# Kernel optimization log

Measured on AMD Instinct MI355X. Metric: run time of the kernel, lower is better.

## Reference

```python
import jax, jax.numpy as jnp
import numpy as np
from jax import lax

IN_CH = 512
OUT_CH = 512
KERNEL = 3
STYLE_DIM = 512
BATCH = 8
HW = 64
EPS = 1e-08
LR_MUL = 1.0


def setup_inputs() -> dict:
    key = jax.random.key(0)
    k1, k2, k3, k4 = jax.random.split(key, 4)
    x = jax.random.normal(k1, (BATCH, IN_CH, HW, HW), dtype=jnp.float32)
    style = jax.random.normal(k2, (BATCH, STYLE_DIM), dtype=jnp.float32)
    weight = jax.random.normal(k3, (1, OUT_CH, IN_CH, KERNEL, KERNEL), dtype=jnp.float32)
    mod_weight = jax.random.normal(k4, (IN_CH, STYLE_DIM), dtype=jnp.float32)
    mod_bias = jnp.ones((IN_CH,), dtype=jnp.float32)  # bias_init=1
    return {"x": x, "style": style, "weight": weight,
            "mod_weight": mod_weight, "mod_bias": mod_bias}


def reference(x, style, weight, mod_weight, mod_bias):
    batch, in_ch, h, w_dim = x.shape
    conv_scale = 1.0 / np.sqrt(in_ch * KERNEL * KERNEL)
    lin_scale = 1.0 / np.sqrt(STYLE_DIM) * LR_MUL

    # EqualizedLinear modulation: style -> per-channel scale, shape (B, in_ch)
    s = style @ (mod_weight * lin_scale).T + mod_bias * LR_MUL

    # Modulate: (B, out, in, k, k)
    w = conv_scale * weight * s[:, None, :, None, None]
    # Demodulate
    demod = lax.rsqrt(jnp.sum(w * w, axis=(2, 3, 4)) + EPS)  # (B, out)
    w = w * demod[:, :, None, None, None]

    pad = KERNEL // 2

    def conv_one(xi, wi):
        # xi: (in, H, W), wi: (out, in, k, k)
        return lax.conv_general_dilated(
            xi[None], wi, window_strides=(1, 1),
            padding=[(pad, pad), (pad, pad)],
            dimension_numbers=("NCHW", "OIHW", "NCHW"))[0]

    out = jax.vmap(conv_one)(x, w)  # (B, out, H, W)
    return out
```

## Files before the change

kernel.cpp:

```cpp
#include <hip/hip_runtime.h>
#include <hip/hip_bf16.h>
#include <cstdint>

#define IN_CH 512
#define OUT_CH 512
#define STYLE_DIM 512
#define BATCH 8
#define HW 64

typedef __bf16 bf16x8 __attribute__((ext_vector_type(8)));
typedef float f32x16 __attribute__((ext_vector_type(16)));

__device__ __forceinline__ void gload_lds16(const void* g, void* l) {
  __builtin_amdgcn_global_load_lds(
      (const __attribute__((address_space(1))) unsigned int*)g,
      (__attribute__((address_space(3))) unsigned int*)l,
      16, 0, 0);
}

#define WAITV(N) asm volatile("s_waitcnt vmcnt(" #N ")" ::: "memory")
#define BARRIER() do { asm volatile("" ::: "memory"); __builtin_amdgcn_s_barrier(); \
                       asm volatile("" ::: "memory"); } while (0)

__global__ void k_style(const float* __restrict__ style, const float* __restrict__ modw,
                        const float* __restrict__ modb, float* __restrict__ s_out,
                        float* __restrict__ zpg) {
  const int tid = threadIdx.x;
  if (blockIdx.x == 128) {
    float4 z = {0.f, 0.f, 0.f, 0.f};
    #pragma unroll
    for (int k = 0; k < 4; ++k) ((float4*)zpg)[tid * 4 + k] = z;
    return;
  }
  __shared__ float st[BATCH * STYLE_DIM];
  for (int i = tid; i < BATCH * STYLE_DIM; i += 256) st[i] = style[i];
  __syncthreads();
  const int ic = blockIdx.x * 4 + (tid >> 6);
  const int l = tid & 63;
  const float* mr = modw + (size_t)ic * STYLE_DIM + l * 8;
  float m[8];
  #pragma unroll
  for (int j = 0; j < 8; ++j) m[j] = mr[j];
  float accs[8];
  #pragma unroll
  for (int b = 0; b < 8; ++b) {
    const float* sb = st + b * STYLE_DIM + l * 8;
    float a = 0.f;
    #pragma unroll
    for (int j = 0; j < 8; ++j) a += m[j] * sb[j];
    accs[b] = a;
  }
  #pragma unroll
  for (int off = 32; off; off >>= 1) {
    #pragma unroll
    for (int b = 0; b < 8; ++b) accs[b] += __shfl_down(accs[b], off, 64);
  }
  if (l == 0) {
    #pragma unroll
    for (int b = 0; b < 8; ++b)
      s_out[b * IN_CH + ic] = accs[b] * 0.04419417382415922f + modb[ic];
  }
}

__global__ void k_prep(const float* __restrict__ x, const float* __restrict__ s,
                       const float* __restrict__ w,
                       __bf16* __restrict__ xgp, __bf16* __restrict__ wgp,
                       float* __restrict__ scale) {
  const int t = threadIdx.x;
  const int bid = blockIdx.x;
  if (bid < 512) {
    const int b = bid >> 6, y = bid & 63;
    const int xcol = t & 63;
    const int g0 = t >> 6;
    const float* sr = s + b * IN_CH;
    const size_t rowbase = ((size_t)(b * 64 + y)) * 8 * 528;
    #pragma unroll
    for (int i = 0; i < 8; ++i) {
      const int g = i * 8 + g0;
      bf16x8 pk;
      #pragma unroll
      for (int e = 0; e < 8; ++e) {
        const int ic = g * 8 + e;
        pk[e] = (__bf16)(x[(((size_t)(b * IN_CH) + ic) * HW + y) * HW + xcol] * sr[ic]);
      }
      const int col = xcol + 1, c = col >> 1;
      const int p = 2 * (((g & 7) + c) & 7) + (col & 1);
      *(bf16x8*)(xgp + (rowbase + (size_t)(g >> 3) * 528 + c * 16 + p) * 8) = pk;
    }
    if (t < 128) {
      const int col = (t & 1) * 65, g = t >> 1;
      const int c = col >> 1;
      const int p = 2 * (((g & 7) + c) & 7) + (col & 1);
      bf16x8 z = {};
      *(bf16x8*)(xgp + (rowbase + (size_t)(g >> 3) * 528 + c * 16 + p) * 8) = z;
    }
  } else if (bid < 1024) {
    const int idx = (bid - 512) * 512 + t;
    const int oc = idx >> 9, ic = idx & 511;
    const int octile = oc >> 8, R = oc & 255, j = R >> 1;
    const int chunk = ic >> 6, sslot = (ic >> 3) & 7, e = ic & 7;
    const int p = 2 * ((sslot + j) & 7) + (R & 1);
    const int u = j * 16 + p;
    const float* pw = w + ((size_t)oc * IN_CH + ic) * 9;
    #pragma unroll
    for (int tp = 0; tp < 9; ++tp)
      wgp[((size_t)((tp * 8 + chunk) * 2 + octile) * 2048 + u) * 8 + e] = (__bf16)pw[tp];
  } else {
    const int oc = (bid - 1024) * 8 + (t >> 6);
    const int l = t & 63;
    float w8[8];
    #pragma unroll
    for (int j = 0; j < 8; ++j) {
      const float* pw = w + ((size_t)oc * IN_CH + l * 8 + j) * 9;
      float sum = 0.f;
      #pragma unroll
      for (int tp = 0; tp < 9; ++tp) { float v = pw[tp]; sum += v * v; }
      w8[j] = sum;
    }
    #pragma unroll
    for (int b = 0; b < 8; ++b) {
      const float* sb = s + b * IN_CH + l * 8;
      float acc = 0.f;
      #pragma unroll
      for (int j = 0; j < 8; ++j) { float sv = sb[j]; acc += sv * sv * w8[j]; }
      #pragma unroll
      for (int off = 32; off; off >>= 1) acc += __shfl_down(acc, off, 64);
      if (l == 0)
        scale[b * OUT_CH + oc] =
            rsqrtf(acc * (1.0f / 4608.0f) + 1e-8f) * 0.014731391274719732f;
    }
  }
}

__global__ __launch_bounds__(512, 2) void k_conv(
    const __bf16* __restrict__ Wgp,
    const __bf16* __restrict__ Xgp,
    const float* __restrict__ scale,
    const __bf16* __restrict__ zpg,
    float* __restrict__ out)
{
  __shared__ __attribute__((aligned(16))) __bf16 Xs[3584 * 8];
  __shared__ __attribute__((aligned(16))) __bf16 Wl[3][2048 * 8];

  const int tid = threadIdx.x;
  const int lane = tid & 63;
  const int wid = tid >> 6;
  const int wm = wid >> 2;
  const int wn = wid & 3;
  const int ln31 = lane & 31;
  const int laneK = lane >> 5;
  const int kord = wid & 3;

  const int bid0 = blockIdx.x;
  const int bid = (bid0 & 7) * 32 + (bid0 >> 3);
  const int octile = bid & 1;
  const int ptile = (bid >> 1) & 15;
  const int b = bid >> 5;
  const int r0 = ptile * 4;
  const int oc0 = octile * 256;

  auto stage_w = [&](int chunkv, int tapv, int bsel) {
    const __bf16* base = Wgp + (size_t)((tapv * 8 + chunkv) * 2 + octile) * (2048 * 8);
    #pragma unroll
    for (int i = 0; i < 4; ++i) {
      const int u = i * 512 + tid;
      gload_lds16(base + (size_t)u * 8, (void*)((char*)Wl[bsel] + u * 16));
    }
  };
  auto stage_x = [&](int chunkv) {
    #pragma unroll
    for (int i = 0; i < 7; ++i) {
      const unsigned u = i * 512 + tid;
      const unsigned row = u / 528u;
      const unsigned rr = u - row * 528u;
      const int y = r0 - 1 + (int)row;
      const bool ok = (u < 3168u) & (y >= 0) & (y < HW);
      const __bf16* src = ok
          ? Xgp + (((size_t)(b * 64 + y) * 8 + chunkv) * 528 + rr) * 8
          : zpg;
      gload_lds16(src, (void*)((char*)Xs + u * 16));
    }
  };

  stage_x(0);
  stage_w(0, 0, 0);
  stage_w(0, 1, 1);

  int aoffR[4];
  #pragma unroll
  for (int i = 0; i < 4; ++i)
    aoffR[i] = ((ln31 + 4 * (kord + i) + 2 * laneK) & 15) * 8;
  int beleR[3][4];
  #pragma unroll
  for (int dxi = 0; dxi < 3; ++dxi) {
    const int col = ln31 + dxi, c = col >> 1;
    #pragma unroll
    for (int i = 0; i < 4; ++i) {
      const int pos = (col & 1) + 2 * ((2 * (kord + i) + laneK + c) & 7);
      beleR[dxi][i] = c * 128 + pos * 8;
    }
  }
  const __bf16* __restrict__ ab0 = Wl[0] + (64 * wm + (ln31 >> 1)) * 128;
  const __bf16* __restrict__ ab1 = Wl[1] + (64 * wm + (ln31 >> 1)) * 128;
  const __bf16* __restrict__ ab2 = Wl[2] + (64 * wm + (ln31 >> 1)) * 128;

  f32x16 acc[4][2] = {};
  bf16x8 bvp0, bvp1;

#define TAPBODY(T) { \
    if ((T) == 8 && c == 7) { WAITV(0); } else { WAITV(4); } \
    BARRIER(); \
    const __bf16* __restrict__ abase = ((T) % 3 == 0) ? ab0 : ((T) % 3 == 1) ? ab1 : ab2; \
    const __bf16* __restrict__ xbase = Xs + (wn + (T) / 3) * (33 * 128); \
    _Pragma("unroll") \
    for (int i = 0; i < 4; ++i) { \
      const int ael = aoffR[i]; \
      const int bel = beleR[(T) % 3][i]; \
      bf16x8 av[4], bv[2]; \
      _Pragma("unroll") \
      for (int mf = 0; mf < 4; ++mf) av[mf] = *(const bf16x8*)(abase + mf * 2048 + ael); \
      if ((T) > 0 && i == 0) { bv[0] = bvp0; bv[1] = bvp1; } \
      else { bv[0] = *(const bf16x8*)(xbase + bel); \
             bv[1] = *(const bf16x8*)(xbase + 2048 + bel); } \
      _Pragma("unroll") \
      for (int mf = 0; mf < 4; ++mf) { \
        acc[mf][0] = __builtin_amdgcn_mfma_f32_32x32x16_bf16(av[mf], bv[0], acc[mf][0], 0, 0, 0); \
        acc[mf][1] = __builtin_amdgcn_mfma_f32_32x32x16_bf16(av[mf], bv[1], acc[mf][1], 0, 0, 0); \
      } \
    } \
    if ((T) < 8) {    \
      const __bf16* __restrict__ xn = Xs + (wn + ((T) + 1) / 3) * (33 * 128); \
      const int beln = beleR[((T) + 1) % 3][0]; \
      bvp0 = *(const bf16x8*)(xn + beln); \
      bvp1 = *(const bf16x8*)(xn + 2048 + beln); \
    } \
    if ((T) == 8) { \
      if (c < 7) { BARRIER(); stage_x(c + 1); stage_w(c + 1, 1, 1); } \
    } else if ((T) <= 6) { \
      stage_w(c, (T) + 2, ((T) + 2) % 3); \
    } else {  \
      if (c < 7) stage_w(c + 1, 0, 0); \
    } \
  }

  #pragma unroll 1
  for (int c = 0; c < 8; ++c) {
    TAPBODY(0) TAPBODY(1) TAPBODY(2)
    TAPBODY(3) TAPBODY(4) TAPBODY(5)
    TAPBODY(6) TAPBODY(7) TAPBODY(8)
  }

  const int y = r0 + wn;
  #pragma unroll
  for (int mf = 0; mf < 4; ++mf) {
    #pragma unroll
    for (int reg = 0; reg < 16; ++reg) {
      const int rowid = (reg & 3) + 8 * (reg >> 2) + 4 * laneK;
      const int oc = oc0 + 128 * wm + 32 * mf + rowid;
      const float sc = scale[b * OUT_CH + oc];
      float* op = out + (((size_t)(b * OUT_CH + oc) * HW + y) * HW) + ln31;
      op[0] = acc[mf][0][reg] * sc;
      op[32] = acc[mf][1][reg] * sc;
    }
  }
}

extern "C" void kernel_launch(void* const* d_in, const int* in_sizes, int n_in,
                              void* d_out, int out_size, void* d_ws, size_t ws_size,
                              hipStream_t stream) {
  const float* x      = (const float*)d_in[0];
  const float* style  = (const float*)d_in[1];
  const float* weight = (const float*)d_in[2];
  const float* modw   = (const float*)d_in[3];
  const float* modb   = (const float*)d_in[4];
  float* out = (float*)d_out;

  char* ws = (char*)d_ws;
  float*  s_buf = (float*)(ws + 0);
  float*  scale = (float*)(ws + 16384);
  __bf16* zpg   = (__bf16*)(ws + 32768);
  __bf16* wgp   = (__bf16*)(ws + 49152);
  __bf16* xgp   = (__bf16*)(ws + 49152 + 9 * 8 * 2 * 2048 * 8 * 2);

  k_style<<<129, 256, 0, stream>>>(style, modw, modb, s_buf, (float*)zpg);
  k_prep<<<1088, 512, 0, stream>>>(x, s_buf, weight, xgp, wgp, scale);
  k_conv<<<256, 512, 0, stream>>>(wgp, xgp, scale, zpg, out);
}
```

Measured before the change: 160.5 us.

## Shrink conv tile to 128 OC with 32-channel K chunks and 4-wave blocks

Reorganizes the implicit-GEMM conv so each block covers 128 output channels with 4 waves (instead of 256 OC with 8 waves), using 32-input-channel chunks instead of 64. The grid doubles to 512 blocks, and the packed X and W layouts in the prep kernel get matching new swizzles. The goal is better occupancy and load balance across the CUs by using smaller LDS tiles. The cost is twice as many barrier-separated K steps, more re-reads of X per output channel, and removal of the B-fragment prefetch across taps.

```diff
diff --git a/kernel.cpp b/kernel.cpp
--- a/kernel.cpp
+++ b/kernel.cpp
@@ -73,7 +73,7 @@
     const int xcol = t & 63;
     const int g0 = t >> 6;
     const float* sr = s + b * IN_CH;
-    const size_t rowbase = ((size_t)(b * 64 + y)) * 8 * 528;
+    const size_t rowbase = ((size_t)(b * 64 + y)) * 16 * 272;
     #pragma unroll
     for (int i = 0; i < 8; ++i) {
       const int g = i * 8 + g0;
@@ -83,28 +83,32 @@
         const int ic = g * 8 + e;
         pk[e] = (__bf16)(x[(((size_t)(b * IN_CH) + ic) * HW + y) * HW + xcol] * sr[ic]);
       }
-      const int col = xcol + 1, c = col >> 1;
-      const int p = 2 * (((g & 7) + c) & 7) + (col & 1);
-      *(bf16x8*)(xgp + (rowbase + (size_t)(g >> 3) * 528 + c * 16 + p) * 8) = pk;
-    }
-    if (t < 128) {
-      const int col = (t & 1) * 65, g = t >> 1;
-      const int c = col >> 1;
-      const int p = 2 * (((g & 7) + c) & 7) + (col & 1);
+      const int col = xcol + 1, c4 = col >> 2;
+      const int p = (col & 3) + 4 * (((g & 3) + c4) & 3);
+      *(bf16x8*)(xgp + (rowbase + (size_t)(g >> 2) * 272 + c4 * 16 + p) * 8) = pk;
+    }
+    if (t < 256) {
+      const int hc = t & 3;
+      const int col = hc ? 64 + hc : 0;
+      const int g = t >> 2;
+      const int c4 = col >> 2;
+      const int p = (col & 3) + 4 * (((g & 3) + c4) & 3);
       bf16x8 z = {};
-      *(bf16x8*)(xgp + (rowbase + (size_t)(g >> 3) * 528 + c * 16 + p) * 8) = z;
+      *(bf16x8*)(xgp + (rowbase + (size_t)(g >> 2) * 272 + c4 * 16 + p) * 8) = z;
     }
   } else if (bid < 1024) {
     const int idx = (bid - 512) * 512 + t;
     const int oc = idx >> 9, ic = idx & 511;
-    const int octile = oc >> 8, R = oc & 255, j = R >> 1;
-    const int chunk = ic >> 6, sslot = (ic >> 3) & 7, e = ic & 7;
-    const int p = 2 * ((sslot + j) & 7) + (R & 1);
+    const int octile = oc >> 7;
+    const int R = oc & 127, j = R >> 2, r = R & 3;
+    const int chunk = ic >> 5;
+    const int sl = (ic >> 3) & 3, e = ic & 7;
+    const int p = r + 4 * ((sl + j) & 3);
     const int u = j * 16 + p;
     const float* pw = w + ((size_t)oc * IN_CH + ic) * 9;
     #pragma unroll
     for (int tp = 0; tp < 9; ++tp)
-      wgp[((size_t)((tp * 8 + chunk) * 2 + octile) * 2048 + u) * 8 + e] = (__bf16)pw[tp];
+      wgp[((size_t)((tp * 16 + chunk) * 4 + octile) * 512 + u) * 8 + e] = (__bf16)pw[tp];
   } else {
     const int oc = (bid - 1024) * 8 + (t >> 6);
     const int l = t & 63;
@@ -132,51 +136,49 @@
   }
 }
 
-__global__ __launch_bounds__(512, 2) void k_conv(
+__global__ __launch_bounds__(256, 2) void k_conv(
     const __bf16* __restrict__ Wgp,
     const __bf16* __restrict__ Xgp,
     const float* __restrict__ scale,
     const __bf16* __restrict__ zpg,
     float* __restrict__ out)
 {
-  __shared__ __attribute__((aligned(16))) __bf16 Xs[3584 * 8];
-  __shared__ __attribute__((aligned(16))) __bf16 Wl[3][2048 * 8];
+  __shared__ __attribute__((aligned(16))) __bf16 Xs[1792 * 8];
+  __shared__ __attribute__((aligned(16))) __bf16 Wl[3][512 * 8];
 
   const int tid = threadIdx.x;
   const int lane = tid & 63;
-  const int wid = tid >> 6;
-  const int wm = wid >> 2;
-  const int wn = wid & 3;
+  const int wn = tid >> 6;
   const int ln31 = lane & 31;
   const int laneK = lane >> 5;
-  const int kord = wid & 3;
 
   const int bid0 = blockIdx.x;
-  const int bid = (bid0 & 7) * 32 + (bid0 >> 3);
-  const int octile = bid & 1;
-  const int ptile = (bid >> 1) & 15;
-  const int b = bid >> 5;
+  const int bid = (bid0 & 7) * 64 + (bid0 >> 3);
+  const int b = bid >> 6;
+  const int rem = bid & 63;
+  const int ptile = rem >> 2;
+  const int octile = rem & 3;
   const int r0 = ptile * 4;
-  const int oc0 = octile * 256;
+  const int oc0 = octile * 128;
 
   auto stage_w = [&](int chunkv, int tapv, int bsel) {
-    const __bf16* base = Wgp + (size_t)((tapv * 8 + chunkv) * 2 + octile) * (2048 * 8);
-    #pragma unroll
-    for (int i = 0; i < 4; ++i) {
-      const int u = i * 512 + tid;
+    const __bf16* base = Wgp + (size_t)((tapv * 16 + chunkv) * 4 + octile) * (512 * 8);
+    #pragma unroll
+    for (int i = 0; i < 2; ++i) {
+      const int u = i * 256 + tid;
       gload_lds16(base + (size_t)u * 8, (void*)((char*)Wl[bsel] + u * 16));
     }
   };
   auto stage_x = [&](int chunkv) {
     #pragma unroll
     for (int i = 0; i < 7; ++i) {
-      const unsigned u = i * 512 + tid;
-      const unsigned row = u / 528u;
-      const unsigned rr = u - row * 528u;
+      const unsigned u = i * 256 + tid;
+      const unsigned row = u / 272u;
+      const unsigned rr = u - row * 272u;
       const int y = r0 - 1 + (int)row;
-      const bool ok = (u < 3168u) & (y >= 0) & (y < HW);
+      const bool ok = (u < 1632u) & (y >= 0) & (y < HW);
       const __bf16* src = ok
-          ? Xgp + (((size_t)(b * 64 + y) * 8 + chunkv) * 528 + rr) * 8
+          ? Xgp + (((size_t)(b * 64 + y) * 16 + chunkv) * 272 + rr) * 8
           : zpg;
       gload_lds16(src, (void*)((char*)Xs + u * 16));
     }
@@ -186,65 +188,58 @@
   stage_w(0, 0, 0);
   stage_w(0, 1, 1);
 
-  int aoffR[4];
-  #pragma unroll
-  for (int i = 0; i < 4; ++i)
-    aoffR[i] = ((ln31 + 4 * (kord + i) + 2 * laneK) & 15) * 8;
-  int beleR[3][4];
+  int aoffR[2];
+  #pragma unroll
+  for (int ksl = 0; ksl < 2; ++ksl)
+    aoffR[ksl] = ((ln31 + 8 * ksl + 4 * laneK) & 15) * 8;
+  int beleR[3][2];
   #pragma unroll
   for (int dxi = 0; dxi < 3; ++dxi) {
-    const int col = ln31 + dxi, c = col >> 1;
-    #pragma unroll
-    for (int i = 0; i < 4; ++i) {
-      const int pos = (col & 1) + 2 * ((2 * (kord + i) + laneK + c) & 7);
-      beleR[dxi][i] = c * 128 + pos * 8;
-    }
-  }
-  const __bf16* __restrict__ ab0 = Wl[0] + (64 * wm + (ln31 >> 1)) * 128;
-  const __bf16* __restrict__ ab1 = Wl[1] + (64 * wm + (ln31 >> 1)) * 128;
-  const __bf16* __restrict__ ab2 = Wl[2] + (64 * wm + (ln31 >> 1)) * 128;
+    const int col = ln31 + dxi;
+    const int c4 = col >> 2;
+    #pragma unroll
+    for (int ksl = 0; ksl < 2; ++ksl) {
+      const int pos = (col + 8 * ksl + 4 * laneK) & 15;
+      beleR[dxi][ksl] = c4 * 128 + pos * 8;
+    }
+  }
+  const __bf16* __restrict__ ab0 = Wl[0] + (ln31 >> 2) * 128;
+  const __bf16* __restrict__ ab1 = Wl[1] + (ln31 >> 2) * 128;
+  const __bf16* __restrict__ ab2 = Wl[2] + (ln31 >> 2) * 128;
 
   f32x16 acc[4][2] = {};
-  bf16x8 bvp0, bvp1;
 
 #define TAPBODY(T) { \
-    if ((T) == 8 && c == 7) { WAITV(0); } else { WAITV(4); } \
+    if ((T) == 8 && c == 15) { WAITV(0); } else { WAITV(2); } \
     BARRIER(); \
     const __bf16* __restrict__ abase = ((T) % 3 == 0) ? ab0 : ((T) % 3 == 1) ? ab1 : ab2; \
-    const __bf16* __restrict__ xbase = Xs + (wn + (T) / 3) * (33 * 128); \
+    const __bf16* __restrict__ xbase = Xs + (wn + (T) / 3) * 2176; \
     _Pragma("unroll") \
-    for (int i = 0; i < 4; ++i) { \
-      const int ael = aoffR[i]; \
-      const int bel = beleR[(T) % 3][i]; \
+    for (int ksl = 0; ksl < 2; ++ksl) { \
+      const int ael = aoffR[ksl]; \
+      const int bel = beleR[(T) % 3][ksl]; \
       bf16x8 av[4], bv[2]; \
       _Pragma("unroll") \
-      for (int mf = 0; mf < 4; ++mf) av[mf] = *(const bf16x8*)(abase + mf * 2048 + ael); \
-      if ((T) > 0 && i == 0) { bv[0] = bvp0; bv[1] = bvp1; } \
-      else { bv[0] = *(const bf16x8*)(xbase + bel); \
-             bv[1] = *(const bf16x8*)(xbase + 2048 + bel); } \
+      for (int mf = 0; mf < 4; ++mf) av[mf] = *(const bf16x8*)(abase + mf * 1024 + ael); \
+      bv[0] = *(const bf16x8*)(xbase + bel); \
+      bv[1] = *(const bf16x8*)(xbase + 1024 + bel); \
       _Pragma("unroll") \
       for (int mf = 0; mf < 4; ++mf) { \
         acc[mf][0] = __builtin_amdgcn_mfma_f32_32x32x16_bf16(av[mf], bv[0], acc[mf][0], 0, 0, 0); \
         acc[mf][1] = __builtin_amdgcn_mfma_f32_32x32x16_bf16(av[mf], bv[1], acc[mf][1], 0, 0, 0); \
       } \
     } \
-    if ((T) < 8) {    \
-      const __bf16* __restrict__ xn = Xs + (wn + ((T) + 1) / 3) * (33 * 128); \
-      const int beln = beleR[((T) + 1) % 3][0]; \
-      bvp0 = *(const bf16x8*)(xn + beln); \
-      bvp1 = *(const bf16x8*)(xn + 2048 + beln); \
-    } \
     if ((T) == 8) { \
-      if (c < 7) { BARRIER(); stage_x(c + 1); stage_w(c + 1, 1, 1); } \
+      if (c < 15) { BARRIER(); stage_x(c + 1); stage_w(c + 1, 1, 1); } \
     } else if ((T) <= 6) { \
       stage_w(c, (T) + 2, ((T) + 2) % 3); \
     } else {  \
-      if (c < 7) stage_w(c + 1, 0, 0); \
+      if (c < 15) stage_w(c + 1, 0, 0); \
     } \
   }
 
   #pragma unroll 1
-  for (int c = 0; c < 8; ++c) {
+  for (int c = 0; c < 16; ++c) {
     TAPBODY(0) TAPBODY(1) TAPBODY(2)
     TAPBODY(3) TAPBODY(4) TAPBODY(5)
     TAPBODY(6) TAPBODY(7) TAPBODY(8)
@@ -256,7 +251,7 @@
     #pragma unroll
     for (int reg = 0; reg < 16; ++reg) {
       const int rowid = (reg & 3) + 8 * (reg >> 2) + 4 * laneK;
-      const int oc = oc0 + 128 * wm + 32 * mf + rowid;
+      const int oc = oc0 + 32 * mf + rowid;
       const float sc = scale[b * OUT_CH + oc];
       float* op = out + (((size_t)(b * OUT_CH + oc) * HW + y) * HW) + ln31;
       op[0] = acc[mf][0][reg] * sc;
@@ -280,9 +275,9 @@
   float*  scale = (float*)(ws + 16384);
   __bf16* zpg   = (__bf16*)(ws + 32768);
   __bf16* wgp   = (__bf16*)(ws + 49152);
-  __bf16* xgp   = (__bf16*)(ws + 49152 + 9 * 8 * 2 * 2048 * 8 * 2);
+  __bf16* xgp   = (__bf16*)(ws + 49152 + 9 * 16 * 4 * 512 * 16);
 
   k_style<<<129, 256, 0, stream>>>(style, modw, modb, s_buf, (float*)zpg);
   k_prep<<<1088, 512, 0, stream>>>(x, s_buf, weight, xgp, wgp, scale);
-  k_conv<<<256, 512, 0, stream>>>(wgp, xgp, scale, zpg, out);
-}
+  k_conv<<<512, 256, 0, stream>>>(wgp, xgp, scale, zpg, out);
+}
```

After: 160.9 us. Within noise of the previous version (+0.2%).

## Load conv input operands straight from global memory instead of staging in LDS

Applied to the files above, without the earlier changes.

The conv kernel stops staging the input tile in shared memory and has each wave read its B-operand fragments directly from a new padded global layout, with the top and bottom halo rows pre-zeroed by extra blocks in the style kernel. Weight staging becomes a uniform rolling schedule across chunks, which removes the extra per-chunk barrier and the input restaging step. This frees LDS and cuts barrier stalls, but in exchange each wave issues more global or L2 loads and has no explicit software prefetch for X, so latency has to be hidden by the wait placement and by occupancy.

```diff
diff --git a/kernel.cpp b/kernel.cpp
--- a/kernel.cpp
+++ b/kernel.cpp
@@ -22,14 +22,28 @@
 #define BARRIER() do { asm volatile("" ::: "memory"); __builtin_amdgcn_s_barrier(); \
                        asm volatile("" ::: "memory"); } while (0)
 
+#define XSLOT 528
+#define XROW  4224
+#define XCHUNK (66 * 4224)
+
 __global__ void k_style(const float* __restrict__ style, const float* __restrict__ modw,
                         const float* __restrict__ modb, float* __restrict__ s_out,
-                        float* __restrict__ zpg) {
+                        __bf16* __restrict__ xgp) {
   const int tid = threadIdx.x;
-  if (blockIdx.x == 128) {
-    float4 z = {0.f, 0.f, 0.f, 0.f};
-    #pragma unroll
-    for (int k = 0; k < 4; ++k) ((float4*)zpg)[tid * 4 + k] = z;
+  if (blockIdx.x >= 128) {
+    const int b = blockIdx.x - 128;
+    bf16x8 z = {};
+    #pragma unroll
+    for (int it = 0; it < 33; ++it) {
+      const int u = it * 256 + tid;
+      const int chunk = u / 1056;
+      const int rem = u - chunk * 1056;
+      const int yidx = (rem / 528) * 65;
+      const int rem2 = rem % 528;
+      const int slot = rem2 / 66, col = rem2 % 66;
+      *(bf16x8*)(xgp + ((size_t)(b * 8 + chunk) * XCHUNK + (size_t)yidx * XROW
+                        + slot * XSLOT + col * 8)) = z;
+    }
     return;
   }
   __shared__ float st[BATCH * STYLE_DIM];
@@ -73,7 +87,6 @@
     const int xcol = t & 63;
     const int g0 = t >> 6;
     const float* sr = s + b * IN_CH;
-    const size_t rowbase = ((size_t)(b * 64 + y)) * 8 * 528;
     #pragma unroll
     for (int i = 0; i < 8; ++i) {
       const int g = i * 8 + g0;
@@ -83,16 +96,14 @@
         const int ic = g * 8 + e;
         pk[e] = (__bf16)(x[(((size_t)(b * IN_CH) + ic) * HW + y) * HW + xcol] * sr[ic]);
       }
-      const int col = xcol + 1, c = col >> 1;
-      const int p = 2 * (((g & 7) + c) & 7) + (col & 1);
-      *(bf16x8*)(xgp + (rowbase + (size_t)(g >> 3) * 528 + c * 16 + p) * 8) = pk;
+      *(bf16x8*)(xgp + ((size_t)(b * 8 + (g >> 3)) * XCHUNK + (size_t)(y + 1) * XROW
+                        + (g & 7) * XSLOT + (xcol + 1) * 8)) = pk;
     }
     if (t < 128) {
       const int col = (t & 1) * 65, g = t >> 1;
-      const int c = col >> 1;
-      const int p = 2 * (((g & 7) + c) & 7) + (col & 1);
       bf16x8 z = {};
-      *(bf16x8*)(xgp + (rowbase + (size_t)(g >> 3) * 528 + c * 16 + p) * 8) = z;
+      *(bf16x8*)(xgp + ((size_t)(b * 8 + (g >> 3)) * XCHUNK + (size_t)(y + 1) * XROW
+                        + (g & 7) * XSLOT + col * 8)) = z;
     }
   } else if (bid < 1024) {
     const int idx = (bid - 512) * 512 + t;
@@ -136,10 +147,8 @@
     const __bf16* __restrict__ Wgp,
     const __bf16* __restrict__ Xgp,
     const float* __restrict__ scale,
-    const __bf16* __restrict__ zpg,
     float* __restrict__ out)
 {
-  __shared__ __attribute__((aligned(16))) __bf16 Xs[3584 * 8];
   __shared__ __attribute__((aligned(16))) __bf16 Wl[3][2048 * 8];
 
   const int tid = threadIdx.x;
@@ -149,7 +158,6 @@
   const int wn = wid & 3;
   const int ln31 = lane & 31;
   const int laneK = lane >> 5;
-  const int kord = wid & 3;
 
   const int bid0 = blockIdx.x;
   const int bid = (bid0 & 7) * 32 + (bid0 >> 3);
@@ -167,80 +175,53 @@
       gload_lds16(base + (size_t)u * 8, (void*)((char*)Wl[bsel] + u * 16));
     }
   };
-  auto stage_x = [&](int chunkv) {
-    #pragma unroll
-    for (int i = 0; i < 7; ++i) {
-      const unsigned u = i * 512 + tid;
-      const unsigned row = u / 528u;
-      const unsigned rr = u - row * 528u;
-      const int y = r0 - 1 + (int)row;
-      const bool ok = (u < 3168u) & (y >= 0) & (y < HW);
-      const __bf16* src = ok
-          ? Xgp + (((size_t)(b * 64 + y) * 8 + chunkv) * 528 + rr) * 8
-          : zpg;
-      gload_lds16(src, (void*)((char*)Xs + u * 16));
-    }
-  };
-
-  stage_x(0);
+
   stage_w(0, 0, 0);
   stage_w(0, 1, 1);
 
-  int aoffR[4];
-  #pragma unroll
-  for (int i = 0; i < 4; ++i)
-    aoffR[i] = ((ln31 + 4 * (kord + i) + 2 * laneK) & 15) * 8;
-  int beleR[3][4];
-  #pragma unroll
-  for (int dxi = 0; dxi < 3; ++dxi) {
-    const int col = ln31 + dxi, c = col >> 1;
-    #pragma unroll
-    for (int i = 0; i < 4; ++i) {
-      const int pos = (col & 1) + 2 * ((2 * (kord + i) + laneK + c) & 7);
-      beleR[dxi][i] = c * 128 + pos * 8;
-    }
-  }
+  int aoff8[4];
+  #pragma unroll
+  for (int ks = 0; ks < 4; ++ks) aoff8[ks] = ((ln31 + 4 * ks + 2 * laneK) & 15) * 8;
   const __bf16* __restrict__ ab0 = Wl[0] + (64 * wm + (ln31 >> 1)) * 128;
   const __bf16* __restrict__ ab1 = Wl[1] + (64 * wm + (ln31 >> 1)) * 128;
   const __bf16* __restrict__ ab2 = Wl[2] + (64 * wm + (ln31 >> 1)) * 128;
+  const __bf16* __restrict__ xrowb =
+      Xgp + (size_t)(b * 8) * XCHUNK + (size_t)(r0 + wn) * XROW + laneK * XSLOT;
+  int bcol[3];
+  #pragma unroll
+  for (int dxi = 0; dxi < 3; ++dxi) bcol[dxi] = (ln31 + dxi) * 8;
 
   f32x16 acc[4][2] = {};
-  bf16x8 bvp0, bvp1;
 
 #define TAPBODY(T) { \
-    if ((T) == 8 && c == 7) { WAITV(0); } else { WAITV(4); } \
+    WAITV(4); \
+    const __bf16* __restrict__ xr = xrowb + ((T) / 3) * XROW + bcol[(T) % 3]; \
+    bf16x8 bv0[4], bv1[4]; \
+    _Pragma("unroll") \
+    for (int ks = 0; ks < 4; ++ks) { \
+      const __bf16* p_ = xr + ks * (2 * XSLOT); \
+      bv0[ks] = *(const bf16x8*)p_; \
+      bv1[ks] = *(const bf16x8*)(p_ + 256); \
+    } \
     BARRIER(); \
+    { \
+      int s2 = c * 9 + (T) + 2, c2 = s2 / 9, t2 = s2 - 9 * c2; \
+      if (s2 >= 72) { c2 = 7; t2 = 8; }    \
+      stage_w(c2, t2, ((T) + 2) % 3); \
+    } \
     const __bf16* __restrict__ abase = ((T) % 3 == 0) ? ab0 : ((T) % 3 == 1) ? ab1 : ab2; \
-    const __bf16* __restrict__ xbase = Xs + (wn + (T) / 3) * (33 * 128); \
     _Pragma("unroll") \
-    for (int i = 0; i < 4; ++i) { \
-      const int ael = aoffR[i]; \
-      const int bel = beleR[(T) % 3][i]; \
-      bf16x8 av[4], bv[2]; \
+    for (int ks = 0; ks < 4; ++ks) { \
+      bf16x8 av[4]; \
       _Pragma("unroll") \
-      for (int mf = 0; mf < 4; ++mf) av[mf] = *(const bf16x8*)(abase + mf * 2048 + ael); \
-      if ((T) > 0 && i == 0) { bv[0] = bvp0; bv[1] = bvp1; } \
-      else { bv[0] = *(const bf16x8*)(xbase + bel); \
-             bv[1] = *(const bf16x8*)(xbase + 2048 + bel); } \
+      for (int mf = 0; mf < 4; ++mf) av[mf] = *(const bf16x8*)(abase + mf * 2048 + aoff8[ks]); \
       _Pragma("unroll") \
       for (int mf = 0; mf < 4; ++mf) { \
-        acc[mf][0] = __builtin_amdgcn_mfma_f32_32x32x16_bf16(av[mf], bv[0], acc[mf][0], 0, 0, 0); \
-        acc[mf][1] = __builtin_amdgcn_mfma_f32_32x32x16_bf16(av[mf], bv[1], acc[mf][1], 0, 0, 0); \
+        acc[mf][0] = __builtin_amdgcn_mfma_f32_32x32x16_bf16(av[mf], bv0[ks], acc[mf][0], 0, 0, 0); \
+        acc[mf][1] = __builtin_amdgcn_mfma_f32_32x32x16_bf16(av[mf], bv1[ks], acc[mf][1], 0, 0, 0); \
       } \
     } \
-    if ((T) < 8) {    \
-      const __bf16* __restrict__ xn = Xs + (wn + ((T) + 1) / 3) * (33 * 128); \
-      const int beln = beleR[((T) + 1) % 3][0]; \
-      bvp0 = *(const bf16x8*)(xn + beln); \
-      bvp1 = *(const bf16x8*)(xn + 2048 + beln); \
-    } \
-    if ((T) == 8) { \
-      if (c < 7) { BARRIER(); stage_x(c + 1); stage_w(c + 1, 1, 1); } \
-    } else if ((T) <= 6) { \
-      stage_w(c, (T) + 2, ((T) + 2) % 3); \
-    } else {  \
-      if (c < 7) stage_w(c + 1, 0, 0); \
-    } \
+    if ((T) == 8) xrowb += XCHUNK; \
   }
 
   #pragma unroll 1
@@ -278,11 +259,10 @@
   char* ws = (char*)d_ws;
   float*  s_buf = (float*)(ws + 0);
   float*  scale = (float*)(ws + 16384);
-  __bf16* zpg   = (__bf16*)(ws + 32768);
-  __bf16* wgp   = (__bf16*)(ws + 49152);
-  __bf16* xgp   = (__bf16*)(ws + 49152 + 9 * 8 * 2 * 2048 * 8 * 2);
-
-  k_style<<<129, 256, 0, stream>>>(style, modw, modb, s_buf, (float*)zpg);
+  __bf16* wgp   = (__bf16*)(ws + 32768);
+  __bf16* xgp   = (__bf16*)(ws + 32768 + 9 * 8 * 2 * 2048 * 8 * 2);
+
+  k_style<<<136, 256, 0, stream>>>(style, modw, modb, s_buf, xgp);
   k_prep<<<1088, 512, 0, stream>>>(x, s_buf, weight, xgp, wgp, scale);
-  k_conv<<<256, 512, 0, stream>>>(wgp, xgp, scale, zpg, out);
-}
+  k_conv<<<256, 512, 0, stream>>>(wgp, xgp, scale, out);
+}
```

Measured after the change: 173.2 us. 1.08x slower.
